# Optimization experiments

Hardware: AMD Instinct MI355X
Metric: run time of the kernel (lower is better)

Reference implementation:

```python
import jax, jax.numpy as jnp
import numpy as np


def setup_inputs() -> dict:
    key = jax.random.key(0)
    k1, k2, k3, k4 = jax.random.split(key, 4)
    B, T, E, D = 4, 4096, 2048, 128
    x = jax.random.normal(k1, (B, T, E), dtype=jnp.float32)
    # nn.Linear(E, D, bias=False): y = x @ W where W is [E, D]
    scale = 1.0 / np.sqrt(E)
    Wq = jax.random.normal(k2, (E, D), dtype=jnp.float32) * scale
    Wk = jax.random.normal(k3, (E, D), dtype=jnp.float32) * scale
    Wv = jax.random.normal(k4, (E, D), dtype=jnp.float32) * scale
    return {"x": x, "Wq": Wq, "Wk": Wk, "Wv": Wv}


def reference(x, Wq, Wk, Wv):
    # Single attention head, prefill path (kv_cache=None, T_q == T_k).
    D = Wq.shape[1]
    Q = jnp.einsum('bte,ed->btd', x, Wq)
    K = jnp.einsum('bte,ed->btd', x, Wk)
    V = jnp.einsum('bte,ed->btd', x, Wv)
    scores = jnp.einsum('bqd,bkd->bqk', Q, K) / jnp.sqrt(jnp.float32(D))
    T = x.shape[1]
    causal = jnp.tril(jnp.ones((T, T), dtype=bool))  # [T_q, T_k]
    scores = jnp.where(causal[None, :, :], scores, -jnp.inf)
    attn = jax.nn.softmax(scores, axis=-1)
    out = jnp.einsum('bqk,bkd->bqd', attn, V)
    return out
```

## Files before the change

kernel.cpp:

```cpp
#include <hip/hip_runtime.h>
#include <hip/hip_bf16.h>

typedef short bf16x8 __attribute__((ext_vector_type(8)));
typedef float f32x4  __attribute__((ext_vector_type(4)));

#define T_SEQ 4096
#define NB    4
#define E_DIM 2048
#define D_DIM 128
#define M_TOT (NB * T_SEQ)
#define NCHUNK 4
#define CHUNK_KT 16
#define SM_SHIFT 12.0f

__device__ __forceinline__ ushort f2bf(float f) {
  union { float f; unsigned u; } c; c.f = f;
  unsigned u = c.u;
  unsigned r = (u + 0x7FFFu + ((u >> 16) & 1u)) >> 16;
  return (ushort)r;
}
__device__ __forceinline__ float bf2f(ushort u) {
  union { unsigned u; float f; } c; c.u = ((unsigned)u) << 16;
  return c.f;
}
__device__ __forceinline__ bf16x8 cvt8(const float4& lo, const float4& hi) {
  union { __hip_bfloat162 h; ushort u[2]; } t;
  union { ushort u[8]; bf16x8 v; } r;
  t.h = __float22bfloat162_rn(make_float2(lo.x, lo.y)); r.u[0] = t.u[0]; r.u[1] = t.u[1];
  t.h = __float22bfloat162_rn(make_float2(lo.z, lo.w)); r.u[2] = t.u[0]; r.u[3] = t.u[1];
  t.h = __float22bfloat162_rn(make_float2(hi.x, hi.y)); r.u[4] = t.u[0]; r.u[5] = t.u[1];
  t.h = __float22bfloat162_rn(make_float2(hi.z, hi.w)); r.u[6] = t.u[0]; r.u[7] = t.u[1];
  return r.v;
}

__device__ __forceinline__ void gl2lds16(const void* g, void* l) {
  __builtin_amdgcn_global_load_lds(
      (const __attribute__((address_space(1))) unsigned int*)g,
      (__attribute__((address_space(3))) unsigned int*)l, 16, 0, 0);
}

__global__ __launch_bounds__(256) void build_wt(const float* __restrict__ Wq,
                                                const float* __restrict__ Wk,
                                                const float* __restrict__ Wv,
                                                ushort* __restrict__ Wt) {
  __shared__ ushort tile[64][72];
  const int tid = threadIdx.x;
  const int k0 = blockIdx.x * 64, n0 = blockIdx.y * 64, o = blockIdx.z;
  const float* W = (o == 0) ? Wq : ((o == 1) ? Wk : Wv);
  for (int i = 0; i < 4; i++) {
    int c = tid + i * 256;
    int r = c >> 4, c4 = (c & 15) * 4;
    float4 v = *(const float4*)(W + (size_t)(k0 + r) * D_DIM + n0 + c4);
    ushort4 b4;
    b4.x = f2bf(v.x); b4.y = f2bf(v.y); b4.z = f2bf(v.z); b4.w = f2bf(v.w);
    *(ushort4*)(&tile[r][c4]) = b4;
  }
  __syncthreads();
  for (int i = 0; i < 2; i++) {
    int c = tid + i * 256;
    int nn = c >> 3, k8 = (c & 7) * 8;
    ushort tmp[8];
    for (int j = 0; j < 8; j++) tmp[j] = tile[k8 + j][nn];
    *(uint4*)(Wt + (size_t)((o << 7) + n0 + nn) * E_DIM + k0 + k8) = *(const uint4*)tmp;
  }
}

__global__ __launch_bounds__(256) void qkv_gemm(const float* __restrict__ x,
                                                const ushort* __restrict__ Wt,
                                                ushort* __restrict__ Q,
                                                ushort* __restrict__ K,
                                                ushort* __restrict__ V) {
  __shared__ ushort Bs[2][192 * 64];

  const int tid  = threadIdx.x;
  const int wave = tid >> 6, lane = tid & 63;
  const int quad = lane >> 4, l16 = lane & 15;
  const int wm = wave >> 1, wn = wave & 1;
  const int m0 = blockIdx.x * 64;
  const int n0 = blockIdx.y * 192;

  f32x4 acc[2][6] = {};

  const int s_   = wave * 64 + lane;
  const int n_   = s_ >> 3, p_ = s_ & 7;

#define DMA_B(k0_, buf_)                                                        \
  _Pragma("unroll")                                                             \
  for (int i_ = 0; i_ < 6; i_++) {                                              \
    int slotbase = i_ * 256 + wave * 64;                                        \
    int n = (i_ * 256 >> 3) + n_;       \
    int cg = p_ ^ (n & 7);                                                      \
    gl2lds16(Wt + (size_t)(n0 + n) * E_DIM + (k0_) + cg * 8,                    \
             (char*)(buf_) + (size_t)slotbase * 16);                            \
  }

#define LOAD_A(k0_, dst)                                                        \
  _Pragma("unroll")                                                             \
  for (int mi_ = 0; mi_ < 2; mi_++)                                             \
    _Pragma("unroll")                                                           \
    for (int kk_ = 0; kk_ < 2; kk_++) {                                         \
      const float* ap_ = xbase + (size_t)mi_ * 16 * E_DIM + (k0_) + kk_ * 32;   \
      dst[mi_][kk_][0] = *(const float4*)ap_;                                   \
      dst[mi_][kk_][1] = *(const float4*)(ap_ + 4);                             \
    }

#define COMPUTE(aBuf, bufidx)                                                   \
  {                                                                             \
    const ushort* bs = Bs[bufidx];                                              \
    _Pragma("unroll")                                                           \
    for (int kk = 0; kk < 2; kk++) {                                            \
      bf16x8 af0 = cvt8(aBuf[0][kk][0], aBuf[0][kk][1]);                        \
      bf16x8 af1 = cvt8(aBuf[1][kk][0], aBuf[1][kk][1]);                        \
      const int sw = ((kk * 4 + quad) ^ (l16 & 7)) * 8;                         \
      _Pragma("unroll")                                                         \
      for (int ni = 0; ni < 6; ni++) {                                          \
        int n = wn * 96 + ni * 16 + l16;                                        \
        bf16x8 bf = *(const bf16x8*)(bs + n * 64 + sw);                         \
        acc[0][ni] = __builtin_amdgcn_mfma_f32_16x16x32_bf16(af0, bf, acc[0][ni], 0, 0, 0); \
        acc[1][ni] = __builtin_amdgcn_mfma_f32_16x16x32_bf16(af1, bf, acc[1][ni], 0, 0, 0); \
      }                                                                         \
    }                                                                           \
  }

  const float* xbase = x + (size_t)(m0 + wm * 32 + l16) * E_DIM + quad * 8;

  float4 a0[2][2][2], a1[2][2][2];

  DMA_B(0, Bs[0]);
  LOAD_A(0, a0);
  asm volatile("s_waitcnt vmcnt(0) lgkmcnt(0)" ::: "memory");
  __builtin_amdgcn_s_barrier();

  for (int it = 0; it < 32; it += 2) {
    DMA_B((it + 1) * 64, Bs[1]);
    LOAD_A((it + 1) * 64, a1);
    asm volatile("s_waitcnt vmcnt(14)" ::: "memory");
    COMPUTE(a0, 0);
    asm volatile("s_waitcnt vmcnt(8) lgkmcnt(0)" ::: "memory");
    __builtin_amdgcn_s_barrier();
    if (it < 30) {
      DMA_B((it + 2) * 64, Bs[0]);
      LOAD_A((it + 2) * 64, a0);
      asm volatile("s_waitcnt vmcnt(14)" ::: "memory");
      COMPUTE(a1, 1);
      asm volatile("s_waitcnt vmcnt(8) lgkmcnt(0)" ::: "memory");
      __builtin_amdgcn_s_barrier();
    } else {
      asm volatile("s_waitcnt vmcnt(0) lgkmcnt(0)" ::: "memory");
      COMPUTE(a1, 1);
    }
  }

  for (int mi = 0; mi < 2; mi++)
    for (int ni = 0; ni < 6; ni++) {
      int colall = n0 + wn * 96 + ni * 16 + l16;
      int o = colall >> 7, d = colall & 127;
      ushort* dst = (o == 0) ? Q : ((o == 1) ? K : V);
      for (int r = 0; r < 4; r++) {
        int row = m0 + wm * 32 + mi * 16 + quad * 4 + r;
        dst[(size_t)row * D_DIM + d] = f2bf(acc[mi][ni][r]);
      }
    }
#undef DMA_B
#undef LOAD_A
#undef COMPUTE
}

__global__ __launch_bounds__(256) void v_transpose(const ushort* __restrict__ V,
                                                   ushort* __restrict__ Vt) {
  __shared__ ushort tile[64][72];
  const int tid = threadIdx.x;
  const int t0 = blockIdx.x * 64, d0 = blockIdx.y * 64, b = blockIdx.z;
  for (int i = 0; i < 2; i++) {
    int c = tid + i * 256;
    int r = c >> 3, cc = (c & 7) * 8;
    *(uint4*)(&tile[r][cc]) = *(const uint4*)(V + (size_t)(b * T_SEQ + t0 + r) * D_DIM + d0 + cc);
  }
  __syncthreads();
  for (int i = 0; i < 2; i++) {
    int c = tid + i * 256;
    int dr = c >> 3, tc = (c & 7) * 8;
    ushort tmp[8];
    for (int j = 0; j < 8; j++) tmp[j] = tile[tc + j][dr];
    *(uint4*)(Vt + (size_t)(b * D_DIM + d0 + dr) * T_SEQ + t0 + tc) = *(const uint4*)tmp;
  }
}

__global__ __launch_bounds__(256) void attn_partial(const ushort* __restrict__ Q,
                                                    const ushort* __restrict__ K,
                                                    const ushort* __restrict__ Vt,
                                                    ushort* __restrict__ Po,
                                                    float* __restrict__ Ll) {
  const int qt = blockIdx.x, cq = blockIdx.y, b = blockIdx.z;
  const int kt0 = cq * CHUNK_KT;
  if (kt0 > qt) return;

  __shared__ ushort Kt[64][136];
  __shared__ ushort Vts[128][72];
  __shared__ ushort Pls[4][16][72];

  const int tid = threadIdx.x;
  const int wave = tid >> 6, lane = tid & 63;
  const int quad = lane >> 4, l16 = lane & 15;

  const int qrow = qt * 64 + wave * 16 + l16;
  bf16x8 qf[4];
  for (int kk = 0; kk < 4; kk++)
    qf[kk] = *(const bf16x8*)(Q + (size_t)(b * T_SEQ + qrow) * D_DIM + kk * 32 + quad * 8);

  bf16x8 ones;
  for (int j = 0; j < 8; j++) ones[j] = (short)0x3F80;

  f32x4 o_acc[8] = {};
  f32x4 lacc = {};
  const float scale2 = 0.08838834764831845f * 1.4426950408889634f;

  const int kt1 = min(qt, kt0 + CHUNK_KT - 1);

  for (int kt = kt0; kt <= kt1; kt++) {
    __syncthreads();
    for (int i = 0; i < 4; i++) {
      int c = tid + i * 256;
      int r = c >> 4, col = (c & 15) * 8;
      *(uint4*)(&Kt[r][col]) = *(const uint4*)(K + (size_t)(b * T_SEQ + kt * 64 + r) * D_DIM + col);
    }
    for (int i = 0; i < 4; i++) {
      int c = tid + i * 256;
      int dr = c >> 3, col = (c & 7) * 8;
      *(uint4*)(&Vts[dr][col]) = *(const uint4*)(Vt + (size_t)(b * D_DIM + dr) * T_SEQ + kt * 64 + col);
    }
    __syncthreads();

    f32x4 s[4] = {};
    for (int kk = 0; kk < 4; kk++) {
      const int kc = kk * 32 + quad * 8;
      for (int ni = 0; ni < 4; ni++) {
        bf16x8 bf = *(const bf16x8*)(&Kt[ni * 16 + l16][kc]);
        s[ni] = __builtin_amdgcn_mfma_f32_16x16x32_bf16(qf[kk], bf, s[ni], 0, 0, 0);
      }
    }
    if (kt == qt) {
      for (int ni = 0; ni < 4; ni++) {
        int kidx = kt * 64 + ni * 16 + l16;
        for (int r = 0; r < 4; r++) {
          int qidx = qt * 64 + wave * 16 + quad * 4 + r;
          float v = (kidx > qidx) ? -1e30f : (s[ni][r] * scale2 - SM_SHIFT);
          s[ni][r] = exp2f(v);
        }
      }
    } else {
      for (int ni = 0; ni < 4; ni++)
        for (int r = 0; r < 4; r++)
          s[ni][r] = exp2f(s[ni][r] * scale2 - SM_SHIFT);
    }
    for (int ni = 0; ni < 4; ni++)
      for (int r = 0; r < 4; r++)
        Pls[wave][quad * 4 + r][ni * 16 + l16] = f2bf(s[ni][r]);
    for (int kk2 = 0; kk2 < 2; kk2++) {
      const int kc = kk2 * 32 + quad * 8;
      bf16x8 pf = *(const bf16x8*)(&Pls[wave][l16][kc]);
      for (int ni = 0; ni < 8; ni++) {
        bf16x8 vf = *(const bf16x8*)(&Vts[ni * 16 + l16][kc]);
        o_acc[ni] = __builtin_amdgcn_mfma_f32_16x16x32_bf16(pf, vf, o_acc[ni], 0, 0, 0);
      }
      lacc = __builtin_amdgcn_mfma_f32_16x16x32_bf16(pf, ones, lacc, 0, 0, 0);
    }
  }

  const int slot = (b * 64 + qt) * NCHUNK + cq;
  for (int ni = 0; ni < 8; ni++)
    for (int r = 0; r < 4; r++) {
      int ql = wave * 16 + quad * 4 + r;
      Po[(size_t)slot * 8192 + ql * D_DIM + ni * 16 + l16] = f2bf(o_acc[ni][r]);
    }
  if (l16 == 0) {
    for (int r = 0; r < 4; r++) {
      int ql = wave * 16 + quad * 4 + r;
      Ll[slot * 64 + ql] = lacc[r];
    }
  }
}

__global__ __launch_bounds__(256) void attn_reduce(const ushort* __restrict__ Po,
                                                   const float* __restrict__ Ll,
                                                   float* __restrict__ out) {
  const int qt = blockIdx.x, b = blockIdx.y;
  const int nc = qt / CHUNK_KT + 1;
  const int tid = threadIdx.x;
  const int row = tid >> 2;
  const int c0  = (tid & 3) * 32;
  const int base_slot = (b * 64 + qt) * NCHUNK;

  float L = 0.f;
  for (int c = 0; c < nc; c++) L += Ll[(base_slot + c) * 64 + row];
  const float inv = 1.0f / L;

  const size_t orow = (size_t)(b * T_SEQ + qt * 64 + row) * D_DIM;
  for (int cc = 0; cc < 32; cc += 8) {
    float a[8] = {0,0,0,0,0,0,0,0};
    for (int c = 0; c < nc; c++) {
      const ushort* p = Po + (size_t)(base_slot + c) * 8192 + row * D_DIM + c0 + cc;
      ushort u[8];
      *(uint4*)u = *(const uint4*)p;
      for (int j = 0; j < 8; j++) a[j] += bf2f(u[j]);
    }
    float4 o0, o1;
    o0.x = a[0] * inv; o0.y = a[1] * inv; o0.z = a[2] * inv; o0.w = a[3] * inv;
    o1.x = a[4] * inv; o1.y = a[5] * inv; o1.z = a[6] * inv; o1.w = a[7] * inv;
    *(float4*)(out + orow + c0 + cc)     = o0;
    *(float4*)(out + orow + c0 + cc + 4) = o1;
  }
}

extern "C" void kernel_launch(void* const* d_in, const int* in_sizes, int n_in,
                              void* d_out, int out_size, void* d_ws, size_t ws_size,
                              hipStream_t stream) {
  const float* x  = (const float*)d_in[0];
  const float* Wq = (const float*)d_in[1];
  const float* Wk = (const float*)d_in[2];
  const float* Wv = (const float*)d_in[3];
  float* out = (float*)d_out;

  ushort* Q  = (ushort*)d_ws;
  ushort* Kb = Q  + (size_t)M_TOT * D_DIM;
  ushort* Vb = Kb + (size_t)M_TOT * D_DIM;
  ushort* Vt = Vb + (size_t)M_TOT * D_DIM;
  ushort* Wt = Vt + (size_t)M_TOT * D_DIM;
  ushort* Po = Wt + (size_t)384 * E_DIM;
  float*  Ll = (float*)(Po + (size_t)NB * 64 * NCHUNK * 8192);

  hipLaunchKernelGGL(build_wt,     dim3(32, 2, 3),       dim3(256), 0, stream, Wq, Wk, Wv, Wt);
  hipLaunchKernelGGL(qkv_gemm,     dim3(256, 2),         dim3(256), 0, stream, x, Wt, Q, Kb, Vb);
  hipLaunchKernelGGL(v_transpose,  dim3(64, 2, 4),       dim3(256), 0, stream, Vb, Vt);
  hipLaunchKernelGGL(attn_partial, dim3(64, NCHUNK, 4),  dim3(256), 0, stream, Q, Kb, Vt, Po, Ll);
  hipLaunchKernelGGL(attn_reduce,  dim3(64, 4),          dim3(256), 0, stream, Po, Ll, out);
}
```

Baseline: 305.8 us.

## Stage converted x tiles in LDS and shrink QKV GEMM N-tile to 96

```diff
diff --git a/kernel.cpp b/kernel.cpp
--- a/kernel.cpp
+++ b/kernel.cpp
@@ -65,95 +65,103 @@
   }
 }
 
-__global__ __launch_bounds__(256) void qkv_gemm(const float* __restrict__ x,
-                                                const ushort* __restrict__ Wt,
-                                                ushort* __restrict__ Q,
-                                                ushort* __restrict__ K,
-                                                ushort* __restrict__ V) {
-  __shared__ ushort Bs[2][192 * 64];
+__global__ __launch_bounds__(256, 4) void qkv_gemm(const float* __restrict__ x,
+                                                   const ushort* __restrict__ Wt,
+                                                   ushort* __restrict__ Q,
+                                                   ushort* __restrict__ K,
+                                                   ushort* __restrict__ V) {
+  __shared__ ushort As[2][64 * 64];
+  __shared__ ushort Bs[2][96 * 64];
 
   const int tid  = threadIdx.x;
   const int wave = tid >> 6, lane = tid & 63;
   const int quad = lane >> 4, l16 = lane & 15;
   const int wm = wave >> 1, wn = wave & 1;
   const int m0 = blockIdx.x * 64;
-  const int n0 = blockIdx.y * 192;
-
-  f32x4 acc[2][6] = {};
-
-  const int s_   = wave * 64 + lane;
-  const int n_   = s_ >> 3, p_ = s_ & 7;
+  const int n0 = blockIdx.y * 96;
+
+  f32x4 acc[2][3] = {};
+
+  const int s_ = wave * 64 + lane;
+  const int n_ = s_ >> 3, p_ = s_ & 7;
+
+  const int ar_ = tid >> 2, aq4_ = tid & 3;
+  const float* xrow = x + (size_t)(m0 + ar_) * E_DIM + aq4_ * 16;
 
 #define DMA_B(k0_, buf_)                                                        \
   _Pragma("unroll")                                                             \
-  for (int i_ = 0; i_ < 6; i_++) {                                              \
+  for (int i_ = 0; i_ < 3; i_++) {                                              \
     int slotbase = i_ * 256 + wave * 64;                                        \
-    int n = (i_ * 256 >> 3) + n_;       \
+    int n = (i_ * 32) + n_;                           \
     int cg = p_ ^ (n & 7);                                                      \
     gl2lds16(Wt + (size_t)(n0 + n) * E_DIM + (k0_) + cg * 8,                    \
              (char*)(buf_) + (size_t)slotbase * 16);                            \
   }
 
-#define LOAD_A(k0_, dst)                                                        \
-  _Pragma("unroll")                                                             \
-  for (int mi_ = 0; mi_ < 2; mi_++)                                             \
-    _Pragma("unroll")                                                           \
-    for (int kk_ = 0; kk_ < 2; kk_++) {                                         \
-      const float* ap_ = xbase + (size_t)mi_ * 16 * E_DIM + (k0_) + kk_ * 32;   \
-      dst[mi_][kk_][0] = *(const float4*)ap_;                                   \
-      dst[mi_][kk_][1] = *(const float4*)(ap_ + 4);                             \
-    }
-
-#define COMPUTE(aBuf, bufidx)                                                   \
+#define GLOAD_A(k0_)                                                            \
   {                                                                             \
-    const ushort* bs = Bs[bufidx];                                              \
+    const float* ap_ = xrow + (k0_);                                            \
+    areg0 = *(const float4*)(ap_);                                              \
+    areg1 = *(const float4*)(ap_ + 4);                                          \
+    areg2 = *(const float4*)(ap_ + 8);                                          \
+    areg3 = *(const float4*)(ap_ + 12);                                         \
+  }
+
+#define CVT_WRITE_A(bufidx)                                                     \
+  {                                                                             \
+    ushort* as_ = As[bufidx];                                                   \
+    bf16x8 w0_ = cvt8(areg0, areg1);                                            \
+    bf16x8 w1_ = cvt8(areg2, areg3);                                            \
+    *(bf16x8*)(as_ + ar_ * 64 + (((aq4_ * 2)     ^ (ar_ & 7)) * 8)) = w0_;      \
+    *(bf16x8*)(as_ + ar_ * 64 + (((aq4_ * 2 + 1) ^ (ar_ & 7)) * 8)) = w1_;      \
+  }
+
+#define COMPUTE(bufidx)                                                         \
+  {                                                                             \
+    const ushort* as_ = As[bufidx];                                             \
+    const ushort* bs_ = Bs[bufidx];                                             \
     _Pragma("unroll")                                                           \
     for (int kk = 0; kk < 2; kk++) {                                            \
-      bf16x8 af0 = cvt8(aBuf[0][kk][0], aBuf[0][kk][1]);                        \
-      bf16x8 af1 = cvt8(aBuf[1][kk][0], aBuf[1][kk][1]);                        \
-      const int sw = ((kk * 4 + quad) ^ (l16 & 7)) * 8;                         \
+      const int slot = ((kk * 4 + quad) ^ (l16 & 7)) * 8;                       \
+      bf16x8 af0 = *(const bf16x8*)(as_ + (wm * 32 + l16) * 64 + slot);         \
+      bf16x8 af1 = *(const bf16x8*)(as_ + (wm * 32 + 16 + l16) * 64 + slot);    \
       _Pragma("unroll")                                                         \
-      for (int ni = 0; ni < 6; ni++) {                                          \
-        int n = wn * 96 + ni * 16 + l16;                                        \
-        bf16x8 bf = *(const bf16x8*)(bs + n * 64 + sw);                         \
+      for (int ni = 0; ni < 3; ni++) {                                          \
+        int n = wn * 48 + ni * 16 + l16;                                        \
+        bf16x8 bf = *(const bf16x8*)(bs_ + n * 64 + slot);                      \
         acc[0][ni] = __builtin_amdgcn_mfma_f32_16x16x32_bf16(af0, bf, acc[0][ni], 0, 0, 0); \
         acc[1][ni] = __builtin_amdgcn_mfma_f32_16x16x32_bf16(af1, bf, acc[1][ni], 0, 0, 0); \
       }                                                                         \
     }                                                                           \
   }
 
-  const float* xbase = x + (size_t)(m0 + wm * 32 + l16) * E_DIM + quad * 8;
-
-  float4 a0[2][2][2], a1[2][2][2];
-
+  float4 areg0, areg1, areg2, areg3;
+
+  GLOAD_A(0);
   DMA_B(0, Bs[0]);
-  LOAD_A(0, a0);
-  asm volatile("s_waitcnt vmcnt(0) lgkmcnt(0)" ::: "memory");
-  __builtin_amdgcn_s_barrier();
+  CVT_WRITE_A(0);
+  __syncthreads();
 
   for (int it = 0; it < 32; it += 2) {
+    GLOAD_A((it + 1) * 64);
     DMA_B((it + 1) * 64, Bs[1]);
-    LOAD_A((it + 1) * 64, a1);
-    asm volatile("s_waitcnt vmcnt(14)" ::: "memory");
-    COMPUTE(a0, 0);
-    asm volatile("s_waitcnt vmcnt(8) lgkmcnt(0)" ::: "memory");
-    __builtin_amdgcn_s_barrier();
+    COMPUTE(0);
+    CVT_WRITE_A(1);
+    __syncthreads();
     if (it < 30) {
+      GLOAD_A((it + 2) * 64);
       DMA_B((it + 2) * 64, Bs[0]);
-      LOAD_A((it + 2) * 64, a0);
-      asm volatile("s_waitcnt vmcnt(14)" ::: "memory");
-      COMPUTE(a1, 1);
-      asm volatile("s_waitcnt vmcnt(8) lgkmcnt(0)" ::: "memory");
-      __builtin_amdgcn_s_barrier();
+      COMPUTE(1);
+      CVT_WRITE_A(0);
+      __syncthreads();
     } else {
-      asm volatile("s_waitcnt vmcnt(0) lgkmcnt(0)" ::: "memory");
-      COMPUTE(a1, 1);
+      COMPUTE(1);
     }
   }
 
   for (int mi = 0; mi < 2; mi++)
-    for (int ni = 0; ni < 6; ni++) {
-      int colall = n0 + wn * 96 + ni * 16 + l16;
+    for (int ni = 0; ni < 3; ni++) {
+      int colall = n0 + wn * 48 + ni * 16 + l16;
       int o = colall >> 7, d = colall & 127;
       ushort* dst = (o == 0) ? Q : ((o == 1) ? K : V);
       for (int r = 0; r < 4; r++) {
@@ -162,7 +170,8 @@
       }
     }
 #undef DMA_B
-#undef LOAD_A
+#undef GLOAD_A
+#undef CVT_WRITE_A
 #undef COMPUTE
 }
 
@@ -330,7 +339,7 @@
   float*  Ll = (float*)(Po + (size_t)NB * 64 * NCHUNK * 8192);
 
   hipLaunchKernelGGL(build_wt,     dim3(32, 2, 3),       dim3(256), 0, stream, Wq, Wk, Wv, Wt);
-  hipLaunchKernelGGL(qkv_gemm,     dim3(256, 2),         dim3(256), 0, stream, x, Wt, Q, Kb, Vb);
+  hipLaunchKernelGGL(qkv_gemm,     dim3(256, 4),         dim3(256), 0, stream, x, Wt, Q, Kb, Vb);
   hipLaunchKernelGGL(v_transpose,  dim3(64, 2, 4),       dim3(256), 0, stream, Vb, Vt);
   hipLaunchKernelGGL(attn_partial, dim3(64, NCHUNK, 4),  dim3(256), 0, stream, Q, Kb, Vt, Po, Ll);
   hipLaunchKernelGGL(attn_reduce,  dim3(64, 4),          dim3(256), 0, stream, Po, Ll, out);
```

Result: faster. 297.7 us (-2.7%).
